# Kernel optimization log

Hardware: AMD Instinct MI355X
Metric: run time of the kernel (lower is better)

Reference implementation:

```python
import jax, jax.numpy as jnp
import numpy as np

B, S, D, UNITS = 4, 512, 256, 128
NEG = -1e9


def setup_inputs() -> dict:
    key = jax.random.key(0)
    k1, k2, k3, k4 = jax.random.split(key, 4)
    values = jax.random.normal(k1, (B, S, D), dtype=jnp.float32)
    Wq = jax.random.normal(k2, (D, UNITS), dtype=jnp.float32) * (1.0 / np.sqrt(D))
    Wv = jax.random.normal(k3, (D, UNITS), dtype=jnp.float32) * (1.0 / np.sqrt(D))
    Vw = jax.random.normal(k4, (UNITS,), dtype=jnp.float32) * (1.0 / np.sqrt(UNITS))
    return {"values": values, "Wq": Wq, "Wv": Wv, "Vw": Vw}


def reference(values, Wq, Wv, Vw):
    # values: [B, S, D]
    query = values @ Wq            # [B, S, U]
    value = values @ Wv            # [B, S, U]
    # additive (Bahdanau) score: V . tanh(q_i + v_j) -> [B, S, S]
    feat = jnp.tanh(query[:, :, None, :] + value[:, None, :, :])  # [B,S,S,U]
    score = jnp.einsum('biju,u->bij', feat, Vw)
    seq_len = values.shape[1]
    causal = jnp.tril(jnp.ones((seq_len, seq_len), dtype=jnp.float32))  # lower-tri = visible
    score = score + (1.0 - causal)[None, :, :] * jnp.asarray(NEG, score.dtype)
    attn = jax.nn.softmax(score, axis=-1)          # [B, S, S]
    context = jnp.matmul(attn, values)             # [B, S, D]
    return context
```

## Files before the change

kernel.cpp:

```cpp
#include <hip/hip_runtime.h>
#include <hip/hip_fp16.h>

#define SEQ 512
#define DIM 256
#define UN  128
#define BSZ 2048
#define CSC 2.8853900817779268f

struct h8 { __half2 a, b, c, d; };

static __device__ __forceinline__ unsigned short f2bf(float x) {
  unsigned u = __float_as_uint(x);
  u += 0x7FFF + ((u >> 16) & 1);
  return (unsigned short)(u >> 16);
}
static __device__ __forceinline__ float bf2f(unsigned short s) {
  return __uint_as_float((unsigned)s << 16);
}

__global__ __launch_bounds__(256) void proj_kernel(
    const float* __restrict__ values, const float* __restrict__ Wq,
    const float* __restrict__ Wv, float* __restrict__ Eq,
    unsigned short* __restrict__ Ev, __half* __restrict__ Vf16) {
  __shared__ float vsm[4 * DIM];
  const int t = threadIdx.x;
  const int r0 = blockIdx.x * 4;
  {
    const int row = t >> 6, c4 = (t & 63) * 4;
    const float4 v = *(const float4*)(values + (r0 + row) * DIM + c4);
    *(float4*)&vsm[row * DIM + c4] = v;
    __half2* vf = (__half2*)(Vf16 + (r0 + row) * DIM + c4);
    vf[0] = __floats2half2_rn(v.x, v.y);
    vf[1] = __floats2half2_rn(v.z, v.w);
  }
  __syncthreads();
  const int half = t >> 7, u = t & 127;
  const float* __restrict__ W = half ? Wv : Wq;
  float acc[4] = {0.f, 0.f, 0.f, 0.f};
  for (int d = 0; d < DIM; d += 4) {
    const float w0 = W[(d + 0) * UN + u], w1 = W[(d + 1) * UN + u];
    const float w2 = W[(d + 2) * UN + u], w3 = W[(d + 3) * UN + u];
#pragma unroll
    for (int k = 0; k < 4; ++k) {
      const float4 v = *(const float4*)&vsm[k * DIM + d];
      acc[k] = fmaf(v.x, w0, acc[k]);
      acc[k] = fmaf(v.y, w1, acc[k]);
      acc[k] = fmaf(v.z, w2, acc[k]);
      acc[k] = fmaf(v.w, w3, acc[k]);
    }
  }
  if (!half) {
#pragma unroll
    for (int k = 0; k < 4; ++k)
      Eq[(r0 + k) * UN + u] = __builtin_amdgcn_exp2f(acc[k] * CSC);
  } else {
    ushort4 o;
    o.x = f2bf(__builtin_amdgcn_exp2f(acc[0] * CSC));
    o.y = f2bf(__builtin_amdgcn_exp2f(acc[1] * CSC));
    o.z = f2bf(__builtin_amdgcn_exp2f(acc[2] * CSC));
    o.w = f2bf(__builtin_amdgcn_exp2f(acc[3] * CSC));
    *(ushort4*)(Ev + (size_t)u * BSZ + r0) = o;
  }
}

__global__ __launch_bounds__(256, 4) void attn_kernel(
    const __half* __restrict__ Vf16, const float* __restrict__ Eq,
    const unsigned short* __restrict__ Ev, const float* __restrict__ Vw,
    float* __restrict__ out) {
  __shared__ float sc[2 * SEQ];
  __shared__ float scp[2 * SEQ];
  __shared__ float part[8 * DIM];
  __shared__ float invs[2];

  const int t = threadIdx.x;
  const int b = blockIdx.x >> 8, p = blockIdx.x & 255;
  const int bS = b * SEQ;
  const int i = p;
  const int ihi = SEQ - 1 - p;
  const int jhi = ihi;

  const float* __restrict__ eql = Eq + (size_t)(bS + i) * UN;
  const float* __restrict__ eqh = Eq + (size_t)(bS + ihi) * UN;

  {
    const int qd = t & 127, jb = qd << 2;
    const int u0 = (t >> 7) << 6;
    float* __restrict__ so = (t >> 7) ? scp : sc;
    const unsigned short* __restrict__ evp = Ev + (size_t)u0 * BSZ + bS + jb;
#define LDE(K) (*(const ushort4*)(evp + (size_t)(K) * BSZ))
    if ((t & 64) == 0) {
      float h0=0.f,h1=0.f,h2=0.f,h3=0.f,l0=0.f,l1=0.f,l2=0.f,l3=0.f;
      ushort4 e0 = LDE(0), e1 = LDE(1), e2 = LDE(2), e3 = LDE(3);
#define PRD(EC, KK) { \
      const float qh = eqh[u0 + (KK)], ql = eql[u0 + (KK)], w = Vw[u0 + (KK)]; \
      const float f0 = bf2f(EC.x), f1 = bf2f(EC.y), f2 = bf2f(EC.z), f3 = bf2f(EC.w); \
      h0 = fmaf(w, __builtin_amdgcn_rcpf(fmaf(qh, f0, 1.f)), h0); \
      h1 = fmaf(w, __builtin_amdgcn_rcpf(fmaf(qh, f1, 1.f)), h1); \
      h2 = fmaf(w, __builtin_amdgcn_rcpf(fmaf(qh, f2, 1.f)), h2); \
      h3 = fmaf(w, __builtin_amdgcn_rcpf(fmaf(qh, f3, 1.f)), h3); \
      l0 = fmaf(w, __builtin_amdgcn_rcpf(fmaf(ql, f0, 1.f)), l0); \
      l1 = fmaf(w, __builtin_amdgcn_rcpf(fmaf(ql, f1, 1.f)), l1); \
      l2 = fmaf(w, __builtin_amdgcn_rcpf(fmaf(ql, f2, 1.f)), l2); \
      l3 = fmaf(w, __builtin_amdgcn_rcpf(fmaf(ql, f3, 1.f)), l3); }
      for (int k = 0; k < 64; k += 4) {
        ushort4 n;
        n = LDE(k + 4); PRD(e0, k + 0); e0 = n;
        n = LDE(k + 5); PRD(e1, k + 1); e1 = n;
        n = LDE(k + 6); PRD(e2, k + 2); e2 = n;
        n = LDE(k + 7); PRD(e3, k + 3); e3 = n;
      }
#undef PRD
      *(float4*)&so[SEQ + jb] = make_float4(h0, h1, h2, h3);
      *(float4*)&so[jb]       = make_float4(l0, l1, l2, l3);
    } else if (jb <= jhi) {
      float h0=0.f,h1=0.f,h2=0.f,h3=0.f;
      ushort4 e0 = LDE(0), e1 = LDE(1), e2 = LDE(2), e3 = LDE(3);
#define PRS(EC, KK) { \
      const float qh = eqh[u0 + (KK)], w = Vw[u0 + (KK)]; \
      h0 = fmaf(w, __builtin_amdgcn_rcpf(fmaf(qh, bf2f(EC.x), 1.f)), h0); \
      h1 = fmaf(w, __builtin_amdgcn_rcpf(fmaf(qh, bf2f(EC.y), 1.f)), h1); \
      h2 = fmaf(w, __builtin_amdgcn_rcpf(fmaf(qh, bf2f(EC.z), 1.f)), h2); \
      h3 = fmaf(w, __builtin_amdgcn_rcpf(fmaf(qh, bf2f(EC.w), 1.f)), h3); }
      for (int k = 0; k < 64; k += 4) {
        ushort4 n;
        n = LDE(k + 4); PRS(e0, k + 0); e0 = n;
        n = LDE(k + 5); PRS(e1, k + 1); e1 = n;
        n = LDE(k + 6); PRS(e2, k + 2); e2 = n;
        n = LDE(k + 7); PRS(e3, k + 3); e3 = n;
      }
#undef PRS
      *(float4*)&so[SEQ + jb] = make_float4(h0, h1, h2, h3);
    }
#undef LDE
  }
  __syncthreads();

  {
    const int w = t >> 6, l = t & 63;
    if (w < 2) {
      const int jmax = (w == 0) ? i : jhi;
      float* __restrict__ r0p = sc + w * SEQ;
      const float* __restrict__ r1p = scp + w * SEQ;
      float m = 1e30f;
      for (int j = l; j <= jmax; j += 64) m = fminf(m, r0p[j] + r1p[j]);
#pragma unroll
      for (int o = 32; o; o >>= 1) m = fminf(m, __shfl_xor(m, o));
      float sum = 0.f;
      for (int j = l; j <= jmax; j += 64) {
        const float pr = __builtin_amdgcn_exp2f((m - (r0p[j] + r1p[j])) * CSC);
        r0p[j] = pr;
        sum += pr;
      }
#pragma unroll
      for (int o = 32; o; o >>= 1) sum += __shfl_xor(sum, o);
      if (l == 0) invs[w] = __builtin_amdgcn_rcpf(sum);
    }
  }
  __syncthreads();

  {
    const int g = t >> 6, l = t & 63;
    const int jo = l >> 5, d8 = (l & 31) << 3;
    float alo[8], ahi[8];
#pragma unroll
    for (int k = 0; k < 8; ++k) { alo[k] = 0.f; ahi[k] = 0.f; }
    int j = 2 * g + jo;
    h8 vc = *(const h8*)(Vf16 + (size_t)(bS + j) * DIM + d8);
    float plc = sc[j], phc = sc[SEQ + j];
    for (; j <= i; j += 8) {
      const int jn = (j + 8 <= jhi) ? j + 8 : jhi;
      const h8 vn = *(const h8*)(Vf16 + (size_t)(bS + jn) * DIM + d8);
      const float pln = sc[jn], phn = sc[SEQ + jn];
      const float2 f0 = __half22float2(vc.a), f1 = __half22float2(vc.b);
      const float2 f2 = __half22float2(vc.c), f3 = __half22float2(vc.d);
      alo[0] = fmaf(plc, f0.x, alo[0]); alo[1] = fmaf(plc, f0.y, alo[1]);
      alo[2] = fmaf(plc, f1.x, alo[2]); alo[3] = fmaf(plc, f1.y, alo[3]);
      alo[4] = fmaf(plc, f2.x, alo[4]); alo[5] = fmaf(plc, f2.y, alo[5]);
      alo[6] = fmaf(plc, f3.x, alo[6]); alo[7] = fmaf(plc, f3.y, alo[7]);
      ahi[0] = fmaf(phc, f0.x, ahi[0]); ahi[1] = fmaf(phc, f0.y, ahi[1]);
      ahi[2] = fmaf(phc, f1.x, ahi[2]); ahi[3] = fmaf(phc, f1.y, ahi[3]);
      ahi[4] = fmaf(phc, f2.x, ahi[4]); ahi[5] = fmaf(phc, f2.y, ahi[5]);
      ahi[6] = fmaf(phc, f3.x, ahi[6]); ahi[7] = fmaf(phc, f3.y, ahi[7]);
      vc = vn; plc = pln; phc = phn;
    }
    for (; j <= jhi; j += 8) {
      const int jn = (j + 8 <= jhi) ? j + 8 : jhi;
      const h8 vn = *(const h8*)(Vf16 + (size_t)(bS + jn) * DIM + d8);
      const float phn = sc[SEQ + jn];
      const float2 f0 = __half22float2(vc.a), f1 = __half22float2(vc.b);
      const float2 f2 = __half22float2(vc.c), f3 = __half22float2(vc.d);
      ahi[0] = fmaf(phc, f0.x, ahi[0]); ahi[1] = fmaf(phc, f0.y, ahi[1]);
      ahi[2] = fmaf(phc, f1.x, ahi[2]); ahi[3] = fmaf(phc, f1.y, ahi[3]);
      ahi[4] = fmaf(phc, f2.x, ahi[4]); ahi[5] = fmaf(phc, f2.y, ahi[5]);
      ahi[6] = fmaf(phc, f3.x, ahi[6]); ahi[7] = fmaf(phc, f3.y, ahi[7]);
      vc = vn; phc = phn;
    }
#pragma unroll
    for (int k = 0; k < 8; ++k) {
      alo[k] += __shfl_xor(alo[k], 32);
      ahi[k] += __shfl_xor(ahi[k], 32);
    }
    if (jo == 0) {
      float* __restrict__ plo_ = &part[(g * 2 + 0) * DIM + d8];
      float* __restrict__ phi_ = &part[(g * 2 + 1) * DIM + d8];
      *(float4*)(plo_ + 0) = make_float4(alo[0], alo[1], alo[2], alo[3]);
      *(float4*)(plo_ + 4) = make_float4(alo[4], alo[5], alo[6], alo[7]);
      *(float4*)(phi_ + 0) = make_float4(ahi[0], ahi[1], ahi[2], ahi[3]);
      *(float4*)(phi_ + 4) = make_float4(ahi[4], ahi[5], ahi[6], ahi[7]);
    }
  }
  __syncthreads();

  {
    const float olo = (part[0 * DIM + t] + part[2 * DIM + t] +
                       part[4 * DIM + t] + part[6 * DIM + t]) * invs[0];
    const float ohi = (part[1 * DIM + t] + part[3 * DIM + t] +
                       part[5 * DIM + t] + part[7 * DIM + t]) * invs[1];
    out[(size_t)(bS + i) * DIM + t] = olo;
    out[(size_t)(bS + ihi) * DIM + t] = ohi;
  }
}

extern "C" void kernel_launch(void* const* d_in, const int* in_sizes, int n_in,
                              void* d_out, int out_size, void* d_ws, size_t ws_size,
                              hipStream_t stream) {
  const float* values = (const float*)d_in[0];
  const float* Wq     = (const float*)d_in[1];
  const float* Wv     = (const float*)d_in[2];
  const float* Vw     = (const float*)d_in[3];
  float* out = (float*)d_out;
  float* Eq = (float*)d_ws;
  unsigned short* Ev = (unsigned short*)(Eq + (size_t)BSZ * UN);
  __half* Vf16 = (__half*)(Ev + (size_t)UN * BSZ);
  proj_kernel<<<dim3(BSZ / 4), 256, 0, stream>>>(values, Wq, Wv, Eq, Ev, Vf16);
  attn_kernel<<<dim3(4 * 256), 256, 0, stream>>>(Vf16, Eq, Ev, Vw, out);
}
```

Baseline: 105.3 us.

## Broadcast query/weights and probabilities via readlane; remap PV loop to 4-wide lanes

In the score phase, each lane now loads one query and weight element up front. The per-k values are broadcast with readlane instead of being reloaded from global memory on every iteration. The probability-times-values phase is remapped so each lane owns 4 output dims and each wave strides rows by 4. Probabilities stay in registers and are broadcast with readlane, which removes per-iteration shared-memory reads and the cross-half shuffle reduction. The low row is zero-padded to a fixed 256-row loop, so short causal rows now do extra multiply-adds in exchange for uniform control flow.

```diff
diff --git a/kernel.cpp b/kernel.cpp
--- a/kernel.cpp
+++ b/kernel.cpp
@@ -7,7 +7,7 @@
 #define BSZ 2048
 #define CSC 2.8853900817779268f
 
-struct h8 { __half2 a, b, c, d; };
+struct h4v { __half2 a, b; };
 
 static __device__ __forceinline__ unsigned short f2bf(float x) {
   unsigned u = __float_as_uint(x);
@@ -16,6 +16,9 @@
 }
 static __device__ __forceinline__ float bf2f(unsigned short s) {
   return __uint_as_float((unsigned)s << 16);
+}
+static __device__ __forceinline__ float rdlane(float v, int k) {
+  return __int_as_float(__builtin_amdgcn_readlane(__float_as_int(v), k));
 }
 
 __global__ __launch_bounds__(256) void proj_kernel(
@@ -73,6 +76,7 @@
   __shared__ float invs[2];
 
   const int t = threadIdx.x;
+  const int lane = t & 63;
   const int b = blockIdx.x >> 8, p = blockIdx.x & 255;
   const int bS = b * SEQ;
   const int i = p;
@@ -81,10 +85,14 @@
 
   const float* __restrict__ eql = Eq + (size_t)(bS + i) * UN;
   const float* __restrict__ eqh = Eq + (size_t)(bS + ihi) * UN;
+  const int u0 = (t >> 7) << 6;
+
+  const float qhv = eqh[u0 + lane];
+  const float qlv = eql[u0 + lane];
+  const float wv  = Vw[u0 + lane];
 
   {
     const int qd = t & 127, jb = qd << 2;
-    const int u0 = (t >> 7) << 6;
     float* __restrict__ so = (t >> 7) ? scp : sc;
     const unsigned short* __restrict__ evp = Ev + (size_t)u0 * BSZ + bS + jb;
 #define LDE(K) (*(const ushort4*)(evp + (size_t)(K) * BSZ))
@@ -92,7 +100,9 @@
       float h0=0.f,h1=0.f,h2=0.f,h3=0.f,l0=0.f,l1=0.f,l2=0.f,l3=0.f;
       ushort4 e0 = LDE(0), e1 = LDE(1), e2 = LDE(2), e3 = LDE(3);
 #define PRD(EC, KK) { \
-      const float qh = eqh[u0 + (KK)], ql = eql[u0 + (KK)], w = Vw[u0 + (KK)]; \
+      const float qh = rdlane(qhv, (KK)); \
+      const float ql = rdlane(qlv, (KK)); \
+      const float w  = rdlane(wv,  (KK)); \
       const float f0 = bf2f(EC.x), f1 = bf2f(EC.y), f2 = bf2f(EC.z), f3 = bf2f(EC.w); \
       h0 = fmaf(w, __builtin_amdgcn_rcpf(fmaf(qh, f0, 1.f)), h0); \
       h1 = fmaf(w, __builtin_amdgcn_rcpf(fmaf(qh, f1, 1.f)), h1); \
@@ -116,7 +126,8 @@
       float h0=0.f,h1=0.f,h2=0.f,h3=0.f;
       ushort4 e0 = LDE(0), e1 = LDE(1), e2 = LDE(2), e3 = LDE(3);
 #define PRS(EC, KK) { \
-      const float qh = eqh[u0 + (KK)], w = Vw[u0 + (KK)]; \
+      const float qh = rdlane(qhv, (KK)); \
+      const float w  = rdlane(wv,  (KK)); \
       h0 = fmaf(w, __builtin_amdgcn_rcpf(fmaf(qh, bf2f(EC.x), 1.f)), h0); \
       h1 = fmaf(w, __builtin_amdgcn_rcpf(fmaf(qh, bf2f(EC.y), 1.f)), h1); \
       h2 = fmaf(w, __builtin_amdgcn_rcpf(fmaf(qh, bf2f(EC.z), 1.f)), h2); \
@@ -136,78 +147,74 @@
   __syncthreads();
 
   {
-    const int w = t >> 6, l = t & 63;
-    if (w < 2) {
-      const int jmax = (w == 0) ? i : jhi;
-      float* __restrict__ r0p = sc + w * SEQ;
-      const float* __restrict__ r1p = scp + w * SEQ;
+    const int w = t >> 6, l = lane;
+    if (w == 0) {
       float m = 1e30f;
-      for (int j = l; j <= jmax; j += 64) m = fminf(m, r0p[j] + r1p[j]);
+      for (int j = l; j <= i; j += 64) m = fminf(m, sc[j] + scp[j]);
 #pragma unroll
       for (int o = 32; o; o >>= 1) m = fminf(m, __shfl_xor(m, o));
       float sum = 0.f;
-      for (int j = l; j <= jmax; j += 64) {
-        const float pr = __builtin_amdgcn_exp2f((m - (r0p[j] + r1p[j])) * CSC);
-        r0p[j] = pr;
-        sum += pr;
+      for (int j = l; j < 256; j += 64) {
+        if (j <= i) {
+          const float pr = __builtin_amdgcn_exp2f((m - (sc[j] + scp[j])) * CSC);
+          sc[j] = pr; sum += pr;
+        } else {
+          sc[j] = 0.f;
+        }
       }
 #pragma unroll
       for (int o = 32; o; o >>= 1) sum += __shfl_xor(sum, o);
-      if (l == 0) invs[w] = __builtin_amdgcn_rcpf(sum);
-    }
-  }
-  __syncthreads();
-
-  {
-    const int g = t >> 6, l = t & 63;
-    const int jo = l >> 5, d8 = (l & 31) << 3;
-    float alo[8], ahi[8];
-#pragma unroll
-    for (int k = 0; k < 8; ++k) { alo[k] = 0.f; ahi[k] = 0.f; }
-    int j = 2 * g + jo;
-    h8 vc = *(const h8*)(Vf16 + (size_t)(bS + j) * DIM + d8);
-    float plc = sc[j], phc = sc[SEQ + j];
-    for (; j <= i; j += 8) {
-      const int jn = (j + 8 <= jhi) ? j + 8 : jhi;
-      const h8 vn = *(const h8*)(Vf16 + (size_t)(bS + jn) * DIM + d8);
-      const float pln = sc[jn], phn = sc[SEQ + jn];
-      const float2 f0 = __half22float2(vc.a), f1 = __half22float2(vc.b);
-      const float2 f2 = __half22float2(vc.c), f3 = __half22float2(vc.d);
-      alo[0] = fmaf(plc, f0.x, alo[0]); alo[1] = fmaf(plc, f0.y, alo[1]);
-      alo[2] = fmaf(plc, f1.x, alo[2]); alo[3] = fmaf(plc, f1.y, alo[3]);
-      alo[4] = fmaf(plc, f2.x, alo[4]); alo[5] = fmaf(plc, f2.y, alo[5]);
-      alo[6] = fmaf(plc, f3.x, alo[6]); alo[7] = fmaf(plc, f3.y, alo[7]);
-      ahi[0] = fmaf(phc, f0.x, ahi[0]); ahi[1] = fmaf(phc, f0.y, ahi[1]);
-      ahi[2] = fmaf(phc, f1.x, ahi[2]); ahi[3] = fmaf(phc, f1.y, ahi[3]);
-      ahi[4] = fmaf(phc, f2.x, ahi[4]); ahi[5] = fmaf(phc, f2.y, ahi[5]);
-      ahi[6] = fmaf(phc, f3.x, ahi[6]); ahi[7] = fmaf(phc, f3.y, ahi[7]);
-      vc = vn; plc = pln; phc = phn;
-    }
-    for (; j <= jhi; j += 8) {
-      const int jn = (j + 8 <= jhi) ? j + 8 : jhi;
-      const h8 vn = *(const h8*)(Vf16 + (size_t)(bS + jn) * DIM + d8);
-      const float phn = sc[SEQ + jn];
-      const float2 f0 = __half22float2(vc.a), f1 = __half22float2(vc.b);
-      const float2 f2 = __half22float2(vc.c), f3 = __half22float2(vc.d);
-      ahi[0] = fmaf(phc, f0.x, ahi[0]); ahi[1] = fmaf(phc, f0.y, ahi[1]);
-      ahi[2] = fmaf(phc, f1.x, ahi[2]); ahi[3] = fmaf(phc, f1.y, ahi[3]);
-      ahi[4] = fmaf(phc, f2.x, ahi[4]); ahi[5] = fmaf(phc, f2.y, ahi[5]);
-      ahi[6] = fmaf(phc, f3.x, ahi[6]); ahi[7] = fmaf(phc, f3.y, ahi[7]);
-      vc = vn; phc = phn;
-    }
-#pragma unroll
-    for (int k = 0; k < 8; ++k) {
-      alo[k] += __shfl_xor(alo[k], 32);
-      ahi[k] += __shfl_xor(ahi[k], 32);
-    }
-    if (jo == 0) {
-      float* __restrict__ plo_ = &part[(g * 2 + 0) * DIM + d8];
-      float* __restrict__ phi_ = &part[(g * 2 + 1) * DIM + d8];
-      *(float4*)(plo_ + 0) = make_float4(alo[0], alo[1], alo[2], alo[3]);
-      *(float4*)(plo_ + 4) = make_float4(alo[4], alo[5], alo[6], alo[7]);
-      *(float4*)(phi_ + 0) = make_float4(ahi[0], ahi[1], ahi[2], ahi[3]);
-      *(float4*)(phi_ + 4) = make_float4(ahi[4], ahi[5], ahi[6], ahi[7]);
-    }
+      if (l == 0) invs[0] = __builtin_amdgcn_rcpf(sum);
+    } else if (w == 1) {
+      float m = 1e30f;
+      for (int j = l; j <= jhi; j += 64) m = fminf(m, sc[SEQ + j] + scp[SEQ + j]);
+#pragma unroll
+      for (int o = 32; o; o >>= 1) m = fminf(m, __shfl_xor(m, o));
+      float sum = 0.f;
+      for (int j = l; j <= jhi; j += 64) {
+        const float pr = __builtin_amdgcn_exp2f((m - (sc[SEQ + j] + scp[SEQ + j])) * CSC);
+        sc[SEQ + j] = pr; sum += pr;
+      }
+#pragma unroll
+      for (int o = 32; o; o >>= 1) sum += __shfl_xor(sum, o);
+      if (l == 0) invs[1] = __builtin_amdgcn_rcpf(sum);
+    }
+  }
+  __syncthreads();
+
+  {
+    const int g = t >> 6;
+    const int d4 = lane << 2;
+    const float plo0 = sc[g + (lane << 2)];
+    const float phi0 = sc[SEQ + g + (lane << 2)];
+    const float phi1 = sc[SEQ + 256 + g + (lane << 2)];
+    float a0=0.f,a1=0.f,a2=0.f,a3=0.f, c0=0.f,c1=0.f,c2=0.f,c3=0.f;
+    const __half* __restrict__ vb = Vf16 + (size_t)bS * DIM + d4;
+    h4v vc = *(const h4v*)(vb + g * DIM);
+#pragma unroll 8
+    for (int k = 0; k < 64; ++k) {
+      const h4v vn = *(const h4v*)(vb + (size_t)(g + 4 * k + 4) * DIM);
+      const float pl = rdlane(plo0, k), ph = rdlane(phi0, k);
+      const float2 f01 = __half22float2(vc.a), f23 = __half22float2(vc.b);
+      a0 = fmaf(pl, f01.x, a0); a1 = fmaf(pl, f01.y, a1);
+      a2 = fmaf(pl, f23.x, a2); a3 = fmaf(pl, f23.y, a3);
+      c0 = fmaf(ph, f01.x, c0); c1 = fmaf(ph, f01.y, c1);
+      c2 = fmaf(ph, f23.x, c2); c3 = fmaf(ph, f23.y, c3);
+      vc = vn;
+    }
+    int k2 = 0;
+#pragma unroll 4
+    for (int j = g + 256; j <= jhi; j += 4, ++k2) {
+      const int jn = (j + 4 <= jhi) ? j + 4 : jhi;
+      const h4v vn = *(const h4v*)(vb + (size_t)jn * DIM);
+      const float ph = rdlane(phi1, k2);
+      const float2 f01 = __half22float2(vc.a), f23 = __half22float2(vc.b);
+      c0 = fmaf(ph, f01.x, c0); c1 = fmaf(ph, f01.y, c1);
+      c2 = fmaf(ph, f23.x, c2); c3 = fmaf(ph, f23.y, c3);
+      vc = vn;
+    }
+    *(float4*)&part[(g * 2 + 0) * DIM + d4] = make_float4(a0, a1, a2, a3);
+    *(float4*)&part[(g * 2 + 1) * DIM + d4] = make_float4(c0, c1, c2, c3);
   }
   __syncthreads();
 
```

New measurement: 111.6 us. +6.0%, slower.

## Split attention into score and MFMA context kernels with fp16 probability matrix

Applied to the files above, without the earlier changes.

Removes the scalar FMA context accumulation from the attention kernel. The normalized probabilities are now written to a global fp16 P matrix, and a new ctx_kernel computes P·V with 16x16x32 fp16 MFMA instructions, using a transposed fp16 copy of values produced by proj_kernel. This brings in matrix-core throughput and causal K truncation per row tile. The cost is an extra launch, a write and read of P through global memory, and fp16 rounding of the probabilities.

```diff
diff --git a/kernel.cpp b/kernel.cpp
--- a/kernel.cpp
+++ b/kernel.cpp
@@ -7,7 +7,9 @@
 #define BSZ 2048
 #define CSC 2.8853900817779268f
 
-struct h8 { __half2 a, b, c, d; };
+typedef _Float16 half8 __attribute__((ext_vector_type(8)));
+typedef float   float4v __attribute__((ext_vector_type(4)));
+struct h4s { __half2 a, b; };
 
 static __device__ __forceinline__ unsigned short f2bf(float x) {
   unsigned u = __float_as_uint(x);
@@ -21,7 +23,7 @@
 __global__ __launch_bounds__(256) void proj_kernel(
     const float* __restrict__ values, const float* __restrict__ Wq,
     const float* __restrict__ Wv, float* __restrict__ Eq,
-    unsigned short* __restrict__ Ev, __half* __restrict__ Vf16) {
+    unsigned short* __restrict__ Ev, _Float16* __restrict__ Vt) {
   __shared__ float vsm[4 * DIM];
   const int t = threadIdx.x;
   const int r0 = blockIdx.x * 4;
@@ -29,11 +31,14 @@
     const int row = t >> 6, c4 = (t & 63) * 4;
     const float4 v = *(const float4*)(values + (r0 + row) * DIM + c4);
     *(float4*)&vsm[row * DIM + c4] = v;
-    __half2* vf = (__half2*)(Vf16 + (r0 + row) * DIM + c4);
-    vf[0] = __floats2half2_rn(v.x, v.y);
-    vf[1] = __floats2half2_rn(v.z, v.w);
   }
   __syncthreads();
+  {
+    h4s o;
+    o.a = __floats2half2_rn(vsm[0 * DIM + t], vsm[1 * DIM + t]);
+    o.b = __floats2half2_rn(vsm[2 * DIM + t], vsm[3 * DIM + t]);
+    *(h4s*)(Vt + (size_t)t * BSZ + r0) = o;
+  }
   const int half = t >> 7, u = t & 127;
   const float* __restrict__ W = half ? Wv : Wq;
   float acc[4] = {0.f, 0.f, 0.f, 0.f};
@@ -63,13 +68,11 @@
   }
 }
 
-__global__ __launch_bounds__(256, 4) void attn_kernel(
-    const __half* __restrict__ Vf16, const float* __restrict__ Eq,
-    const unsigned short* __restrict__ Ev, const float* __restrict__ Vw,
-    float* __restrict__ out) {
+__global__ __launch_bounds__(256, 4) void score_kernel(
+    const float* __restrict__ Eq, const unsigned short* __restrict__ Ev,
+    const float* __restrict__ Vw, _Float16* __restrict__ P) {
   __shared__ float sc[2 * SEQ];
   __shared__ float scp[2 * SEQ];
-  __shared__ float part[8 * DIM];
   __shared__ float invs[2];
 
   const int t = threadIdx.x;
@@ -159,66 +162,39 @@
   __syncthreads();
 
   {
-    const int g = t >> 6, l = t & 63;
-    const int jo = l >> 5, d8 = (l & 31) << 3;
-    float alo[8], ahi[8];
-#pragma unroll
-    for (int k = 0; k < 8; ++k) { alo[k] = 0.f; ahi[k] = 0.f; }
-    int j = 2 * g + jo;
-    h8 vc = *(const h8*)(Vf16 + (size_t)(bS + j) * DIM + d8);
-    float plc = sc[j], phc = sc[SEQ + j];
-    for (; j <= i; j += 8) {
-      const int jn = (j + 8 <= jhi) ? j + 8 : jhi;
-      const h8 vn = *(const h8*)(Vf16 + (size_t)(bS + jn) * DIM + d8);
-      const float pln = sc[jn], phn = sc[SEQ + jn];
-      const float2 f0 = __half22float2(vc.a), f1 = __half22float2(vc.b);
-      const float2 f2 = __half22float2(vc.c), f3 = __half22float2(vc.d);
-      alo[0] = fmaf(plc, f0.x, alo[0]); alo[1] = fmaf(plc, f0.y, alo[1]);
-      alo[2] = fmaf(plc, f1.x, alo[2]); alo[3] = fmaf(plc, f1.y, alo[3]);
-      alo[4] = fmaf(plc, f2.x, alo[4]); alo[5] = fmaf(plc, f2.y, alo[5]);
-      alo[6] = fmaf(plc, f3.x, alo[6]); alo[7] = fmaf(plc, f3.y, alo[7]);
-      ahi[0] = fmaf(phc, f0.x, ahi[0]); ahi[1] = fmaf(phc, f0.y, ahi[1]);
-      ahi[2] = fmaf(phc, f1.x, ahi[2]); ahi[3] = fmaf(phc, f1.y, ahi[3]);
-      ahi[4] = fmaf(phc, f2.x, ahi[4]); ahi[5] = fmaf(phc, f2.y, ahi[5]);
-      ahi[6] = fmaf(phc, f3.x, ahi[6]); ahi[7] = fmaf(phc, f3.y, ahi[7]);
-      vc = vn; plc = pln; phc = phn;
-    }
-    for (; j <= jhi; j += 8) {
-      const int jn = (j + 8 <= jhi) ? j + 8 : jhi;
-      const h8 vn = *(const h8*)(Vf16 + (size_t)(bS + jn) * DIM + d8);
-      const float phn = sc[SEQ + jn];
-      const float2 f0 = __half22float2(vc.a), f1 = __half22float2(vc.b);
-      const float2 f2 = __half22float2(vc.c), f3 = __half22float2(vc.d);
-      ahi[0] = fmaf(phc, f0.x, ahi[0]); ahi[1] = fmaf(phc, f0.y, ahi[1]);
-      ahi[2] = fmaf(phc, f1.x, ahi[2]); ahi[3] = fmaf(phc, f1.y, ahi[3]);
-      ahi[4] = fmaf(phc, f2.x, ahi[4]); ahi[5] = fmaf(phc, f2.y, ahi[5]);
-      ahi[6] = fmaf(phc, f3.x, ahi[6]); ahi[7] = fmaf(phc, f3.y, ahi[7]);
-      vc = vn; phc = phn;
-    }
-#pragma unroll
-    for (int k = 0; k < 8; ++k) {
-      alo[k] += __shfl_xor(alo[k], 32);
-      ahi[k] += __shfl_xor(ahi[k], 32);
-    }
-    if (jo == 0) {
-      float* __restrict__ plo_ = &part[(g * 2 + 0) * DIM + d8];
-      float* __restrict__ phi_ = &part[(g * 2 + 1) * DIM + d8];
-      *(float4*)(plo_ + 0) = make_float4(alo[0], alo[1], alo[2], alo[3]);
-      *(float4*)(plo_ + 4) = make_float4(alo[4], alo[5], alo[6], alo[7]);
-      *(float4*)(phi_ + 0) = make_float4(ahi[0], ahi[1], ahi[2], ahi[3]);
-      *(float4*)(phi_ + 4) = make_float4(ahi[4], ahi[5], ahi[6], ahi[7]);
-    }
-  }
-  __syncthreads();
-
-  {
-    const float olo = (part[0 * DIM + t] + part[2 * DIM + t] +
-                       part[4 * DIM + t] + part[6 * DIM + t]) * invs[0];
-    const float ohi = (part[1 * DIM + t] + part[3 * DIM + t] +
-                       part[5 * DIM + t] + part[7 * DIM + t]) * invs[1];
-    out[(size_t)(bS + i) * DIM + t] = olo;
-    out[(size_t)(bS + ihi) * DIM + t] = ohi;
-  }
+    const float invLo = invs[0], invHi = invs[1];
+    const int t2 = t + 256;
+    const float pLo = (t <= i) ? sc[t] * invLo : 0.f;
+    const float pHa = sc[SEQ + t] * invHi;
+    const float pHb = (t2 <= jhi) ? sc[SEQ + t2] * invHi : 0.f;
+    P[(size_t)(bS + i) * SEQ + t]    = (_Float16)pLo;
+    P[(size_t)(bS + ihi) * SEQ + t]  = (_Float16)pHa;
+    P[(size_t)(bS + ihi) * SEQ + t2] = (_Float16)pHb;
+  }
+}
+
+__global__ __launch_bounds__(256) void ctx_kernel(
+    const _Float16* __restrict__ P, const _Float16* __restrict__ Vt,
+    float* __restrict__ out) {
+  const int t = threadIdx.x, lane = t & 63, g = t >> 6;
+  const int x = blockIdx.x;
+  const int b = x >> 7, ri = (x >> 2) & 31, cg = x & 3;
+  const int bS = b * SEQ;
+  const int d0 = cg * 64 + g * 16;
+  const int m = lane & 15, q = lane >> 4;
+  const int Kmax = 16 * ri + 16;
+
+  const _Float16* __restrict__ pA = P  + (size_t)(bS + 16 * ri + m) * SEQ + q * 8;
+  const _Float16* __restrict__ pB = Vt + (size_t)(d0 + m) * BSZ + bS + q * 8;
+  float4v acc = {0.f, 0.f, 0.f, 0.f};
+  for (int k0 = 0; k0 < Kmax; k0 += 32) {
+    const half8 a  = *(const half8*)(pA + k0);
+    const half8 bv = *(const half8*)(pB + k0);
+    acc = __builtin_amdgcn_mfma_f32_16x16x32_f16(a, bv, acc, 0, 0, 0);
+  }
+  float* __restrict__ o = out + (size_t)(bS + 16 * ri + q * 4) * DIM + d0 + m;
+#pragma unroll
+  for (int r = 0; r < 4; ++r) o[(size_t)r * DIM] = acc[r];
 }
 
 extern "C" void kernel_launch(void* const* d_in, const int* in_sizes, int n_in,
@@ -231,7 +207,9 @@
   float* out = (float*)d_out;
   float* Eq = (float*)d_ws;
   unsigned short* Ev = (unsigned short*)(Eq + (size_t)BSZ * UN);
-  __half* Vf16 = (__half*)(Ev + (size_t)UN * BSZ);
-  proj_kernel<<<dim3(BSZ / 4), 256, 0, stream>>>(values, Wq, Wv, Eq, Ev, Vf16);
-  attn_kernel<<<dim3(4 * 256), 256, 0, stream>>>(Vf16, Eq, Ev, Vw, out);
-}
+  _Float16* Vt = (_Float16*)(Ev + (size_t)UN * BSZ);
+  _Float16* P  = Vt + (size_t)DIM * BSZ;
+  proj_kernel<<<dim3(BSZ / 4), 256, 0, stream>>>(values, Wq, Wv, Eq, Ev, Vt);
+  score_kernel<<<dim3(4 * 256), 256, 0, stream>>>(Eq, Ev, Vw, P);
+  ctx_kernel<<<dim3(4 * 32 * 4), 256, 0, stream>>>(P, Vt, out);
+}
```

New measurement: 98.18 us. 1.07x faster.
